# Kernel optimization log

Measured on AMD Instinct MI355X. Metric: run time of the kernel, lower is better.

The kernel has to match this reference:

```python
import jax, jax.numpy as jnp
import numpy as np

B, S, H, F, E, K = 2, 1024, 1024, 4096, 8, 2
TOPK_RATIO = 0.55
EPS = 1e-8


def _ste(x, q):
    # straight-through estimator: forward = q, backward = identity on x
    return x + jax.lax.stop_gradient(q - x)


def ternary_weight(w):
    # BitNet b1.58 absmean ternarization: W -> clip(round(W/mean|W|), -1, 1) * mean|W|
    s = jnp.maximum(jnp.mean(jnp.abs(w)), EPS)
    q = jnp.clip(jnp.round(w / s), -1.0, 1.0) * s
    return _ste(w, q)


def quant_act_int4(x):
    # per-token symmetric int4 fake-quant (range [-7, 7]) with STE
    s = jnp.maximum(jnp.max(jnp.abs(x), axis=-1, keepdims=True), EPS) / 7.0
    q = jnp.clip(jnp.round(x / s), -7.0, 7.0) * s
    return _ste(x, q)


def quant_act_topk_int8(x, ratio):
    # keep top ceil(ratio*d) values by magnitude per token, then int8 fake-quant
    d = x.shape[-1]
    k = int(np.ceil(ratio * d))
    thresh = jax.lax.top_k(jnp.abs(x), k)[0][..., -1:]
    xm = jnp.where(jnp.abs(x) >= thresh, x, 0.0)
    s = jnp.maximum(jnp.max(jnp.abs(xm), axis=-1, keepdims=True), EPS) / 127.0
    q = jnp.clip(jnp.round(xm / s), -127.0, 127.0) * s
    return _ste(xm, q)


def quant_weight_int8(w):
    # per-tensor absmax int8 fake-quant for the router (Int8Linear) with STE
    s = jnp.maximum(jnp.max(jnp.abs(w)), EPS) / 127.0
    q = jnp.clip(jnp.round(w / s), -127.0, 127.0) * s
    return _ste(w, q)


def setup_inputs() -> dict:
    key = jax.random.key(0)
    ks = jax.random.split(key, 5)
    x = jax.random.normal(ks[0], (B, S, H), jnp.float32)
    w_gate = jax.random.normal(ks[1], (E, F, H), jnp.float32) * 0.02
    w_up = jax.random.normal(ks[2], (E, F, H), jnp.float32) * 0.02
    w_down = jax.random.normal(ks[3], (E, H, F), jnp.float32) * 0.02
    w_router = jax.random.normal(ks[4], (E, H), jnp.float32) * 0.02
    return {"x": x, "w_gate": w_gate, "w_up": w_up, "w_down": w_down, "w_router": w_router}


def reference(x, w_gate, w_up, w_down, w_router):
    T = B * S
    xf = x.reshape(T, H)

    # --- router (Int8Linear, higher precision than ternary) ---
    logits = xf @ quant_weight_int8(w_router).T          # [T, E]
    probs = jax.nn.softmax(logits, axis=-1)
    gates, idx = jax.lax.top_k(probs, K)                  # [T, K]
    gates = gates / jnp.sum(gates, axis=-1, keepdims=True)
    # dense combine weights [T, E]
    comb = jnp.zeros((T, E), x.dtype).at[jnp.arange(T)[:, None], idx].set(gates)

    # --- experts: BitFFN (SwiGLU with ternary weights + quantized activations) ---
    xq = quant_act_int4(xf)                               # shared int4 input quant

    def expert(wg, wu, wd):
        g = xq @ ternary_weight(wg).T                     # [T, F]
        u = xq @ ternary_weight(wu).T                     # [T, F]
        h = jax.nn.silu(g) * u
        hq = quant_act_topk_int8(h, TOPK_RATIO)
        return hq @ ternary_weight(wd).T                  # [T, H]

    expert_out = jax.vmap(expert)(w_gate, w_up, w_down)   # [E, T, H]
    out = jnp.einsum('te,eth->th', comb, expert_out)      # gated combine
    return out.reshape(B, S, H)
```

## Files before the change

### kernel.cpp

```cpp
#include <hip/hip_runtime.h>
#include <cstdint>
#include <cstddef>


#define T_TOK 2048
#define HDIM  1024
#define FDIM  4096
#define NEXP  8
#define FH    (FDIM * HDIM)
#define KTOP  2253
#define EPSF  1e-8f
#define PPAD  4608

typedef int v4i  __attribute__((ext_vector_type(4)));
typedef int v16i __attribute__((ext_vector_type(16)));

__global__ __launch_bounds__(256) void k_wabs(const float* __restrict__ w,
                                              float* __restrict__ partials) {
  int m = blockIdx.x, blk = blockIdx.y, tid = threadIdx.x;
  const float4* p = (const float4*)(w + (size_t)m * FH + (size_t)blk * 32768) + tid;
  float s0 = 0.f, s1 = 0.f, s2 = 0.f, s3 = 0.f;
#pragma unroll
  for (int i = 0; i < 8; i++) {
    float4 a = p[(4 * i + 0) * 256];
    float4 b = p[(4 * i + 1) * 256];
    float4 c = p[(4 * i + 2) * 256];
    float4 d = p[(4 * i + 3) * 256];
    s0 += fabsf(a.x) + fabsf(a.y) + fabsf(a.z) + fabsf(a.w);
    s1 += fabsf(b.x) + fabsf(b.y) + fabsf(b.z) + fabsf(b.w);
    s2 += fabsf(c.x) + fabsf(c.y) + fabsf(c.z) + fabsf(c.w);
    s3 += fabsf(d.x) + fabsf(d.y) + fabsf(d.z) + fabsf(d.w);
  }
  float s = (s0 + s1) + (s2 + s3);
  for (int o = 32; o > 0; o >>= 1) s += __shfl_down(s, o);
  __shared__ float lds[4];
  if ((tid & 63) == 0) lds[tid >> 6] = s;
  __syncthreads();
  if (tid == 0) partials[m * 128 + blk] = lds[0] + lds[1] + lds[2] + lds[3];
}

__global__ __launch_bounds__(128) void k_scales8(const float* __restrict__ partials,
                                                 float* __restrict__ s8,
                                                 float* __restrict__ thr8) {
  int tid = threadIdx.x;
  __shared__ float acc[2];
  __shared__ float svals[8];
  for (int m = 0; m < 8; m++) {
    float v = partials[m * 128 + tid];
    for (int o = 32; o > 0; o >>= 1) v += __shfl_down(v, o);
    if ((tid & 63) == 0) acc[tid >> 6] = v;
    __syncthreads();
    if (tid == 0) svals[m] = fmaxf((acc[0] + acc[1]) / (float)FH, EPSF);
    __syncthreads();
  }
  if (tid < 8) {
    float s = svals[tid];
    s8[tid] = s;
    unsigned int lo = 0u, hi = __float_as_uint(s);
    for (int it = 0; it < 32; ++it) {
      unsigned int mid = (lo + hi) >> 1;
      if (mid == lo) break;
      if (__uint_as_float(mid) / s <= 0.5f) lo = mid; else hi = mid;
    }
    thr8[tid] = __uint_as_float(lo);
  }
}

__global__ __launch_bounds__(256) void k_router(const float* __restrict__ wr,
                                                float* __restrict__ wrq) {
  int tid = threadIdx.x;
  __shared__ float lds[4];
  __shared__ float sbc;
  float mx = 0.f;
  for (int i = tid; i < NEXP * HDIM; i += 256) mx = fmaxf(mx, fabsf(wr[i]));
  for (int o = 32; o > 0; o >>= 1) mx = fmaxf(mx, __shfl_down(mx, o));
  if ((tid & 63) == 0) lds[tid >> 6] = mx;
  __syncthreads();
  if (tid == 0)
    sbc = fmaxf(fmaxf(fmaxf(lds[0], lds[1]), fmaxf(lds[2], lds[3])), EPSF) / 127.0f;
  __syncthreads();
  float s = sbc;
  for (int i = tid; i < NEXP * HDIM; i += 256) {
    float q = fminf(fmaxf(rintf(wr[i] / s), -127.f), 127.f);
    wrq[i] = q * s;
  }
}

template <int KD, int RD>
__global__ __launch_bounds__(256) void k_pack(const float* __restrict__ w,
                                              signed char* __restrict__ q,
                                              const float* __restrict__ thr8) {
  constexpr int GR = RD / 32, CCH = KD / 32;
  int e = blockIdx.x / GR, g = blockIdx.x % GR, sl = blockIdx.y;
  float thr = thr8[e];
  __shared__ unsigned int lds[32][257];
  int tid = threadIdx.x;
  const float* wb = w + ((size_t)e * RD + (size_t)g * 32) * KD + (size_t)sl * 1024;
#pragma unroll 4
  for (int i = 0; i < 32; i++) {
    float4 v = *(const float4*)(wb + (size_t)i * KD + tid * 4);
    unsigned int b0 = (fabsf(v.x) > thr) ? ((__float_as_uint(v.x) >> 31) ? 0xFFu : 1u) : 0u;
    unsigned int b1 = (fabsf(v.y) > thr) ? ((__float_as_uint(v.y) >> 31) ? 0xFFu : 1u) : 0u;
    unsigned int b2 = (fabsf(v.z) > thr) ? ((__float_as_uint(v.z) >> 31) ? 0xFFu : 1u) : 0u;
    unsigned int b3 = (fabsf(v.w) > thr) ? ((__float_as_uint(v.w) >> 31) ? 0xFFu : 1u) : 0u;
    lds[i][tid] = b0 | (b1 << 8) | (b2 << 16) | (b3 << 24);
  }
  __syncthreads();
  size_t obase = ((size_t)(e * GR + g) * CCH + (size_t)sl * 32) * 1024;
#pragma unroll
  for (int i2 = 0; i2 < 8; i2++) {
    int mI = i2 * 256 + tid;
    int c = mI >> 6, l2 = mI & 63, ln = l2 & 31, kh = l2 >> 5;
    uint4 d = *(const uint4*)&lds[ln][c * 8 + kh * 4];
    *(uint4*)(q + obase + (size_t)c * 1024 + (size_t)l2 * 16) = d;
  }
}

__global__ __launch_bounds__(256) void k_act_router(const float* __restrict__ x,
                                                    const float* __restrict__ wrq,
                                                    signed char* __restrict__ xq,
                                                    float* __restrict__ sx,
                                                    int* __restrict__ tok_e,
                                                    float* __restrict__ tok_g,
                                                    int* __restrict__ cnt) {
  int t = blockIdx.x, tid = threadIdx.x;
  float4 xv = *(const float4*)(x + (size_t)t * HDIM + tid * 4);
  __shared__ float lds[4];
  __shared__ float sbc;
  __shared__ float part[8][256];
  __shared__ float lg[8];
  float mx = fmaxf(fmaxf(fabsf(xv.x), fabsf(xv.y)), fmaxf(fabsf(xv.z), fabsf(xv.w)));
  for (int o = 32; o > 0; o >>= 1) mx = fmaxf(mx, __shfl_down(mx, o));
  if ((tid & 63) == 0) lds[tid >> 6] = mx;
  __syncthreads();
  if (tid == 0)
    sbc = fmaxf(fmaxf(fmaxf(lds[0], lds[1]), fmaxf(lds[2], lds[3])), EPSF) / 7.0f;
  __syncthreads();
  float s = sbc;
  int q0 = (int)fminf(fmaxf(rintf(xv.x / s), -7.f), 7.f);
  int q1 = (int)fminf(fmaxf(rintf(xv.y / s), -7.f), 7.f);
  int q2 = (int)fminf(fmaxf(rintf(xv.z / s), -7.f), 7.f);
  int q3 = (int)fminf(fmaxf(rintf(xv.w / s), -7.f), 7.f);
  int packed = (q0 & 255) | ((q1 & 255) << 8) | ((q2 & 255) << 16) | (q3 << 24);
  *(int*)(xq + (size_t)t * HDIM + tid * 4) = packed;
  if (tid == 0) sx[t] = s;
#pragma unroll
  for (int e = 0; e < 8; e++) {
    float4 w = *(const float4*)(wrq + e * HDIM + tid * 4);
    part[e][tid] = xv.x * w.x + xv.y * w.y + xv.z * w.z + xv.w * w.w;
  }
  __syncthreads();
  if (tid < 8) {
    float sum = 0.f;
    for (int i = 0; i < 256; i++) sum += part[tid][i];
    lg[tid] = sum;
  }
  __syncthreads();
  if (tid == 0) {
    float m = lg[0];
    for (int e = 1; e < 8; e++) m = fmaxf(m, lg[e]);
    float p[8]; float S = 0.f;
    for (int e = 0; e < 8; e++) { p[e] = expf(lg[e] - m); S += p[e]; }
    for (int e = 0; e < 8; e++) p[e] /= S;
    int e0 = 0;
    for (int e = 1; e < 8; e++) if (p[e] > p[e0]) e0 = e;
    int e1 = -1;
    for (int e = 0; e < 8; e++) { if (e == e0) continue; if (e1 < 0 || p[e] > p[e1]) e1 = e; }
    float g0 = p[e0], g1 = p[e1], gs = g0 + g1;
    tok_e[2 * t] = e0;  tok_e[2 * t + 1] = e1;
    tok_g[2 * t] = g0 / gs;  tok_g[2 * t + 1] = g1 / gs;
    atomicAdd(&cnt[e0], 1); atomicAdd(&cnt[e1], 1);
  }
}

__global__ void k_plan(const int* __restrict__ cnt, int* __restrict__ offs,
                       int* __restrict__ tile_e, int* __restrict__ tile_m0,
                       int* __restrict__ tile_cnt) {
  if (threadIdx.x == 0 && blockIdx.x == 0) {
    int o = 0;
    for (int e = 0; e < 8; e++) { offs[e] = o; o += (cnt[e] + 63) & ~63; }
    offs[8] = o;
    int tt = 0;
    for (int e = 0; e < 8; e++)
      for (int m0 = 0; m0 < cnt[e]; m0 += 64) { tile_e[tt] = e; tile_m0[tt] = m0; tt++; }
    *tile_cnt = tt;
  }
}

__global__ __launch_bounds__(256) void k_scatter(const int* __restrict__ tok_e,
                                                 const float* __restrict__ tok_g,
                                                 const float* __restrict__ sx,
                                                 const int* __restrict__ offs,
                                                 int* __restrict__ cnt2,
                                                 int* __restrict__ pair_tok,
                                                 float* __restrict__ pair_gate,
                                                 float* __restrict__ pair_sx) {
  int t = blockIdx.x * 256 + threadIdx.x;
  if (t >= T_TOK) return;
  for (int k = 0; k < 2; k++) {
    int e = tok_e[2 * t + k];
    int pos = offs[e] + atomicAdd(&cnt2[e], 1);
    pair_tok[pos] = t;
    pair_gate[pos] = tok_g[2 * t + k];
    pair_sx[pos] = sx[t];
  }
}

__global__ __launch_bounds__(256) void k_packA(const int* __restrict__ pair_tok,
                                               const signed char* __restrict__ xq,
                                               signed char* __restrict__ xqp) {
  int idx = blockIdx.x * 256 + threadIdx.x;
  int l = idx & 63, c = (idx >> 6) & 31, pgrp = idx >> 11;
  int p = pgrp * 32 + (l & 31);
  int tok = pair_tok[p];
  const signed char* src = xq + (size_t)tok * HDIM + c * 32 + (l >> 5) * 16;
  *(int4*)(xqp + (size_t)idx * 16) = *(const int4*)src;
}

__global__ __launch_bounds__(256) void k_gemm_gu(const signed char* __restrict__ xqp,
                                                 const signed char* __restrict__ wgp,
                                                 const signed char* __restrict__ wup,
                                                 const int* __restrict__ tile_e,
                                                 const int* __restrict__ tile_m0,
                                                 const int* __restrict__ tile_cnt,
                                                 const int* __restrict__ cnt,
                                                 const int* __restrict__ offs,
                                                 const float* __restrict__ pair_sx,
                                                 const float* __restrict__ s_w,
                                                 unsigned short* __restrict__ hbuf) {
  int bx = blockIdx.x;
  if (bx >= *tile_cnt) return;
  int e = tile_e[bx], m0 = tile_m0[bx];
  int cnt_e = cnt[e], pbase = offs[e];
  int tid = threadIdx.x;
  int wave = tid >> 6, lane = tid & 63, ln = lane & 31, kh = lane >> 5;
  int fgrp = blockIdx.y * 4 + wave;
  const signed char* bg = wgp + (((size_t)e * 128 + fgrp) * 32) * 1024 + lane * 16;
  const signed char* bu = wup + (((size_t)e * 128 + fgrp) * 32) * 1024 + lane * 16;
  const signed char* ap = xqp + ((size_t)((pbase + m0) >> 5) * 32) * 1024 + lane * 16;
  v16i accg0 = {0}, accg1 = {0}, accu0 = {0}, accu1 = {0};
#pragma unroll 8
  for (int c = 0; c < 32; c++) {
    v4i a0 = *(const v4i*)(ap + c * 1024);
    v4i a1 = *(const v4i*)(ap + 32768 + c * 1024);
    v4i b0 = *(const v4i*)(bg + c * 1024);
    v4i b1 = *(const v4i*)(bu + c * 1024);
    accg0 = __builtin_amdgcn_mfma_i32_32x32x32_i8(a0, b0, accg0, 0, 0, 0);
    accg1 = __builtin_amdgcn_mfma_i32_32x32x32_i8(a1, b0, accg1, 0, 0, 0);
    accu0 = __builtin_amdgcn_mfma_i32_32x32x32_i8(a0, b1, accu0, 0, 0, 0);
    accu1 = __builtin_amdgcn_mfma_i32_32x32x32_i8(a1, b1, accu1, 0, 0, 0);
  }
  float sg = s_w[e], su = s_w[8 + e];
  int col = blockIdx.y * 128 + wave * 32 + ln;
#pragma unroll
  for (int r = 0; r < 16; r++) {
    int rr = (r & 3) + 8 * (r >> 2) + 4 * kh;
#pragma unroll
    for (int mt = 0; mt < 2; mt++) {
      int ml = m0 + mt * 32 + rr;
      if (ml < cnt_e) {
        int p = pbase + ml;
        float sxv = pair_sx[p];
        int gi = (mt == 0) ? accg0[r] : accg1[r];
        int ui = (mt == 0) ? accu0[r] : accu1[r];
        float gf = (float)gi * (sxv * sg);
        float uf = (float)ui * (sxv * su);
        float h = gf / (1.0f + expf(-gf)) * uf;
        ((_Float16*)hbuf)[(size_t)p * FDIM + col] = (_Float16)h;
      }
    }
  }
}

__global__ __launch_bounds__(256) void k_select(const unsigned short* __restrict__ hbuf,
                                                signed char* __restrict__ hqp,
                                                const float* __restrict__ pair_gate,
                                                float* __restrict__ pair_f) {
  int wv = threadIdx.x >> 6, lane = threadIdx.x & 63;
  int p = blockIdx.x * 4 + wv;
  const unsigned short* row = hbuf + (size_t)p * FDIM + lane * 64;
  unsigned short hs[64];
#pragma unroll
  for (int i = 0; i < 8; i++)
    *(uint4*)(hs + i * 8) = *(const uint4*)(row + i * 8);
  unsigned short ua[64];
  unsigned int mxb = 0;
#pragma unroll
  for (int j = 0; j < 64; j++) {
    unsigned int u = hs[j] & 0x7fffu;
    ua[j] = (unsigned short)u;
    mxb = (u > mxb) ? u : mxb;
  }
  for (int o = 32; o > 0; o >>= 1) {
    unsigned int t = (unsigned int)__shfl_down((int)mxb, o);
    mxb = (t > mxb) ? t : mxb;
  }
  mxb = (unsigned int)__shfl((int)mxb, 0);
  unsigned int lo = 0, hi = 0x7c00u;
  for (int it = 0; it < 15; ++it) {
    unsigned int mid = (lo + hi) >> 1;
    int cnt = 0;
#pragma unroll
    for (int j = 0; j < 64; j++)
      cnt += (int)__popcll(__ballot((unsigned int)ua[j] >= mid));
    if (cnt >= KTOP) lo = mid; else hi = mid;
  }
  unsigned int thr = lo;
  unsigned short mxs = (unsigned short)mxb;
  float smax = (float)(*(const _Float16*)&mxs);
  float sq = fmaxf(smax, EPSF) / 127.0f;
  int pgrp = p >> 5, ln = p & 31;
#pragma unroll
  for (int gj = 0; gj < 4; gj++) {
    int c = 2 * lane + (gj >> 1);
    int kh = gj & 1;
    signed char outb[16];
#pragma unroll
    for (int t = 0; t < 16; t++) {
      int j = gj * 16 + t;
      float v = (float)(((const _Float16*)hs)[j]);
      float m = ((unsigned int)ua[j] >= thr) ? v : 0.0f;
      float q = fminf(fmaxf(rintf(m / sq), -127.f), 127.f);
      outb[t] = (signed char)(int)q;
    }
    *(int4*)(hqp + ((size_t)((size_t)pgrp * 128 + c) * 64 + kh * 32 + ln) * 16) =
        *(const int4*)outb;
  }
  if (lane == 0) pair_f[p] = pair_gate[p] * sq;
}

__global__ __launch_bounds__(256) void k_gemm_down(const signed char* __restrict__ hqp,
                                                   const signed char* __restrict__ wdp,
                                                   const int* __restrict__ tile_e,
                                                   const int* __restrict__ tile_m0,
                                                   const int* __restrict__ tile_cnt,
                                                   const int* __restrict__ cnt,
                                                   const int* __restrict__ offs,
                                                   const int* __restrict__ pair_tok,
                                                   const float* __restrict__ pair_f,
                                                   const float* __restrict__ s_w,
                                                   float* __restrict__ out) {
  int bx = blockIdx.x;
  if (bx >= *tile_cnt) return;
  int e = tile_e[bx], m0 = tile_m0[bx];
  int cnt_e = cnt[e], pbase = offs[e];
  int tid = threadIdx.x;
  int wave = tid >> 6, lane = tid & 63, ln = lane & 31, kh = lane >> 5;
  int grp_n = blockIdx.y * 4 + wave;
  const signed char* bp = wdp + (((size_t)e * 32 + grp_n) * 128) * 1024 + lane * 16;
  const signed char* ap = hqp + ((size_t)((pbase + m0) >> 5) * 128) * 1024 + lane * 16;
  v16i acc0 = {0}, acc1 = {0};
#pragma unroll 8
  for (int c = 0; c < 128; c++) {
    v4i a0 = *(const v4i*)(ap + (size_t)c * 1024);
    v4i a1 = *(const v4i*)(ap + 131072 + (size_t)c * 1024);
    v4i b  = *(const v4i*)(bp + (size_t)c * 1024);
    acc0 = __builtin_amdgcn_mfma_i32_32x32x32_i8(a0, b, acc0, 0, 0, 0);
    acc1 = __builtin_amdgcn_mfma_i32_32x32x32_i8(a1, b, acc1, 0, 0, 0);
  }
  float sd = s_w[16 + e];
  int col = blockIdx.y * 128 + wave * 32 + ln;
#pragma unroll
  for (int r = 0; r < 16; r++) {
    int rr = (r & 3) + 8 * (r >> 2) + 4 * kh;
#pragma unroll
    for (int mt = 0; mt < 2; mt++) {
      int ml = m0 + mt * 32 + rr;
      if (ml < cnt_e) {
        int p = pbase + ml;
        int ai = (mt == 0) ? acc0[r] : acc1[r];
        float v = (float)ai * (pair_f[p] * sd);
        atomicAdd(out + (size_t)pair_tok[p] * HDIM + col, v);
      }
    }
  }
}

extern "C" void kernel_launch(void* const* d_in, const int* in_sizes, int n_in,
                              void* d_out, int out_size, void* d_ws, size_t ws_size,
                              hipStream_t stream) {
  const float* x  = (const float*)d_in[0];
  const float* wg = (const float*)d_in[1];
  const float* wu = (const float*)d_in[2];
  const float* wd = (const float*)d_in[3];
  const float* wr = (const float*)d_in[4];
  float* out = (float*)d_out;
  char* ws = (char*)d_ws;
  (void)in_sizes; (void)n_in; (void)out_size; (void)ws_size;

  size_t o = 0;
  auto alloc = [&](size_t b) { size_t r = o; o += (b + 255) & ~(size_t)255; return r; };
  float* partials   = (float*)(ws + alloc(3 * 8 * 128 * 4));
  float* s_w        = (float*)(ws + alloc(24 * 4));
  float* thr_w      = (float*)(ws + alloc(24 * 4));
  float* wrq        = (float*)(ws + alloc((size_t)NEXP * HDIM * 4));
  int*   tok_e      = (int*)  (ws + alloc((size_t)T_TOK * 2 * 4));
  float* tok_g      = (float*)(ws + alloc((size_t)T_TOK * 2 * 4));
  int*   cnt        = (int*)  (ws + alloc(256));
  int*   cnt2       = cnt + 8;
  int*   offs       = (int*)  (ws + alloc(16 * 4));
  int*   tile_e     = (int*)  (ws + alloc(128 * 4));
  int*   tile_m0    = (int*)  (ws + alloc(128 * 4));
  int*   tile_cnt   = (int*)  (ws + alloc(4));
  int*   pair_tok   = (int*)  (ws + alloc((size_t)PPAD * 4));
  float* pair_gate  = (float*)(ws + alloc((size_t)PPAD * 4));
  float* pair_sx    = (float*)(ws + alloc((size_t)PPAD * 4));
  float* pair_f     = (float*)(ws + alloc((size_t)PPAD * 4));
  float* sx         = (float*)(ws + alloc((size_t)T_TOK * 4));
  signed char* xq   = (signed char*)(ws + alloc((size_t)T_TOK * HDIM));
  signed char* xqp  = (signed char*)(ws + alloc((size_t)PPAD * HDIM));
  signed char* wgp  = (signed char*)(ws + alloc((size_t)NEXP * FH));
  signed char* wup  = (signed char*)(ws + alloc((size_t)NEXP * FH));
  signed char* wdp  = (signed char*)(ws + alloc((size_t)NEXP * FH));
  unsigned short* hbuf = (unsigned short*)(ws + alloc((size_t)PPAD * FDIM * 2));
  signed char* hqp  = (signed char*)(ws + alloc((size_t)PPAD * FDIM));

  hipMemsetAsync(cnt, 0, 64, stream);
  hipMemsetAsync(pair_tok, 0, (size_t)PPAD * 4, stream);
  hipMemsetAsync(out, 0, (size_t)T_TOK * HDIM * 4, stream);

  k_wabs<<<dim3(8, 128), 256, 0, stream>>>(wg, partials);
  k_scales8<<<1, 128, 0, stream>>>(partials, s_w, thr_w);
  k_pack<1024, 4096><<<dim3(1024, 1), 256, 0, stream>>>(wg, wgp, thr_w);

  k_wabs<<<dim3(8, 128), 256, 0, stream>>>(wu, partials + 1024);
  k_scales8<<<1, 128, 0, stream>>>(partials + 1024, s_w + 8, thr_w + 8);
  k_pack<1024, 4096><<<dim3(1024, 1), 256, 0, stream>>>(wu, wup, thr_w + 8);

  k_wabs<<<dim3(8, 128), 256, 0, stream>>>(wd, partials + 2048);
  k_scales8<<<1, 128, 0, stream>>>(partials + 2048, s_w + 16, thr_w + 16);
  k_pack<4096, 1024><<<dim3(256, 4), 256, 0, stream>>>(wd, wdp, thr_w + 16);

  k_router<<<1, 256, 0, stream>>>(wr, wrq);
  k_act_router<<<T_TOK, 256, 0, stream>>>(x, wrq, xq, sx, tok_e, tok_g, cnt);
  k_plan<<<1, 64, 0, stream>>>(cnt, offs, tile_e, tile_m0, tile_cnt);
  k_scatter<<<8, 256, 0, stream>>>(tok_e, tok_g, sx, offs, cnt2, pair_tok, pair_gate, pair_sx);
  k_packA<<<PPAD / 4, 256, 0, stream>>>(pair_tok, xq, xqp);
  k_gemm_gu<<<dim3(72, 32), 256, 0, stream>>>(xqp, wgp, wup, tile_e, tile_m0, tile_cnt,
                                              cnt, offs, pair_sx, s_w, hbuf);
  k_select<<<PPAD / 4, 256, 0, stream>>>(hbuf, hqp, pair_gate, pair_f);
  k_gemm_down<<<dim3(72, 8), 256, 0, stream>>>(hqp, wdp, tile_e, tile_m0, tile_cnt,
                                               cnt, offs, pair_tok, pair_f, s_w, out);
}
```

Baseline: 810.5 us.

## Enlarge MoE GEMM row tiles to 128 tokens and split down-proj K

```diff
diff --git a/kernel.cpp b/kernel.cpp
--- a/kernel.cpp
+++ b/kernel.cpp
@@ -10,7 +10,7 @@
 #define FH    (FDIM * HDIM)
 #define KTOP  2253
 #define EPSF  1e-8f
-#define PPAD  4608
+#define PPAD  5120
 
 typedef int v4i  __attribute__((ext_vector_type(4)));
 typedef int v16i __attribute__((ext_vector_type(16)));
@@ -178,11 +178,11 @@
                        int* __restrict__ tile_cnt) {
   if (threadIdx.x == 0 && blockIdx.x == 0) {
     int o = 0;
-    for (int e = 0; e < 8; e++) { offs[e] = o; o += (cnt[e] + 63) & ~63; }
+    for (int e = 0; e < 8; e++) { offs[e] = o; o += (cnt[e] + 127) & ~127; }
     offs[8] = o;
     int tt = 0;
     for (int e = 0; e < 8; e++)
-      for (int m0 = 0; m0 < cnt[e]; m0 += 64) { tile_e[tt] = e; tile_m0[tt] = m0; tt++; }
+      for (int m0 = 0; m0 < cnt[e]; m0 += 128) { tile_e[tt] = e; tile_m0[tt] = m0; tt++; }
     *tile_cnt = tt;
   }
 }
@@ -217,17 +217,17 @@
   *(int4*)(xqp + (size_t)idx * 16) = *(const int4*)src;
 }
 
-__global__ __launch_bounds__(256) void k_gemm_gu(const signed char* __restrict__ xqp,
-                                                 const signed char* __restrict__ wgp,
-                                                 const signed char* __restrict__ wup,
-                                                 const int* __restrict__ tile_e,
-                                                 const int* __restrict__ tile_m0,
-                                                 const int* __restrict__ tile_cnt,
-                                                 const int* __restrict__ cnt,
-                                                 const int* __restrict__ offs,
-                                                 const float* __restrict__ pair_sx,
-                                                 const float* __restrict__ s_w,
-                                                 unsigned short* __restrict__ hbuf) {
+__global__ __launch_bounds__(256, 2) void k_gemm_gu(const signed char* __restrict__ xqp,
+                                                    const signed char* __restrict__ wgp,
+                                                    const signed char* __restrict__ wup,
+                                                    const int* __restrict__ tile_e,
+                                                    const int* __restrict__ tile_m0,
+                                                    const int* __restrict__ tile_cnt,
+                                                    const int* __restrict__ cnt,
+                                                    const int* __restrict__ offs,
+                                                    const float* __restrict__ pair_sx,
+                                                    const float* __restrict__ s_w,
+                                                    unsigned short* __restrict__ hbuf) {
   int bx = blockIdx.x;
   if (bx >= *tile_cnt) return;
   int e = tile_e[bx], m0 = tile_m0[bx];
@@ -238,33 +238,34 @@
   const signed char* bg = wgp + (((size_t)e * 128 + fgrp) * 32) * 1024 + lane * 16;
   const signed char* bu = wup + (((size_t)e * 128 + fgrp) * 32) * 1024 + lane * 16;
   const signed char* ap = xqp + ((size_t)((pbase + m0) >> 5) * 32) * 1024 + lane * 16;
-  v16i accg0 = {0}, accg1 = {0}, accu0 = {0}, accu1 = {0};
-#pragma unroll 8
+  v16i acc[4][2] = {};
+#pragma unroll 2
   for (int c = 0; c < 32; c++) {
-    v4i a0 = *(const v4i*)(ap + c * 1024);
-    v4i a1 = *(const v4i*)(ap + 32768 + c * 1024);
-    v4i b0 = *(const v4i*)(bg + c * 1024);
-    v4i b1 = *(const v4i*)(bu + c * 1024);
-    accg0 = __builtin_amdgcn_mfma_i32_32x32x32_i8(a0, b0, accg0, 0, 0, 0);
-    accg1 = __builtin_amdgcn_mfma_i32_32x32x32_i8(a1, b0, accg1, 0, 0, 0);
-    accu0 = __builtin_amdgcn_mfma_i32_32x32x32_i8(a0, b1, accu0, 0, 0, 0);
-    accu1 = __builtin_amdgcn_mfma_i32_32x32x32_i8(a1, b1, accu1, 0, 0, 0);
+    v4i a[4];
+#pragma unroll
+    for (int mg = 0; mg < 4; mg++)
+      a[mg] = *(const v4i*)(ap + (size_t)(mg * 32 + c) * 1024);
+    v4i b0 = *(const v4i*)(bg + (size_t)c * 1024);
+    v4i b1 = *(const v4i*)(bu + (size_t)c * 1024);
+#pragma unroll
+    for (int mg = 0; mg < 4; mg++) {
+      acc[mg][0] = __builtin_amdgcn_mfma_i32_32x32x32_i8(a[mg], b0, acc[mg][0], 0, 0, 0);
+      acc[mg][1] = __builtin_amdgcn_mfma_i32_32x32x32_i8(a[mg], b1, acc[mg][1], 0, 0, 0);
+    }
   }
   float sg = s_w[e], su = s_w[8 + e];
   int col = blockIdx.y * 128 + wave * 32 + ln;
 #pragma unroll
-  for (int r = 0; r < 16; r++) {
-    int rr = (r & 3) + 8 * (r >> 2) + 4 * kh;
-#pragma unroll
-    for (int mt = 0; mt < 2; mt++) {
-      int ml = m0 + mt * 32 + rr;
+  for (int mg = 0; mg < 4; mg++) {
+#pragma unroll
+    for (int r = 0; r < 16; r++) {
+      int rr = (r & 3) + 8 * (r >> 2) + 4 * kh;
+      int ml = m0 + mg * 32 + rr;
       if (ml < cnt_e) {
         int p = pbase + ml;
         float sxv = pair_sx[p];
-        int gi = (mt == 0) ? accg0[r] : accg1[r];
-        int ui = (mt == 0) ? accu0[r] : accu1[r];
-        float gf = (float)gi * (sxv * sg);
-        float uf = (float)ui * (sxv * su);
+        float gf = (float)acc[mg][0][r] * (sxv * sg);
+        float uf = (float)acc[mg][1][r] * (sxv * su);
         float h = gf / (1.0f + expf(-gf)) * uf;
         ((_Float16*)hbuf)[(size_t)p * FDIM + col] = (_Float16)h;
       }
@@ -299,11 +300,11 @@
   unsigned int lo = 0, hi = 0x7c00u;
   for (int it = 0; it < 15; ++it) {
     unsigned int mid = (lo + hi) >> 1;
-    int cnt = 0;
+    int cntk = 0;
 #pragma unroll
     for (int j = 0; j < 64; j++)
-      cnt += (int)__popcll(__ballot((unsigned int)ua[j] >= mid));
-    if (cnt >= KTOP) lo = mid; else hi = mid;
+      cntk += (int)__popcll(__ballot((unsigned int)ua[j] >= mid));
+    if (cntk >= KTOP) lo = mid; else hi = mid;
   }
   unsigned int thr = lo;
   unsigned short mxs = (unsigned short)mxb;
@@ -329,47 +330,50 @@
   if (lane == 0) pair_f[p] = pair_gate[p] * sq;
 }
 
-__global__ __launch_bounds__(256) void k_gemm_down(const signed char* __restrict__ hqp,
-                                                   const signed char* __restrict__ wdp,
-                                                   const int* __restrict__ tile_e,
-                                                   const int* __restrict__ tile_m0,
-                                                   const int* __restrict__ tile_cnt,
-                                                   const int* __restrict__ cnt,
-                                                   const int* __restrict__ offs,
-                                                   const int* __restrict__ pair_tok,
-                                                   const float* __restrict__ pair_f,
-                                                   const float* __restrict__ s_w,
-                                                   float* __restrict__ out) {
+__global__ __launch_bounds__(256, 2) void k_gemm_down(const signed char* __restrict__ hqp,
+                                                      const signed char* __restrict__ wdp,
+                                                      const int* __restrict__ tile_e,
+                                                      const int* __restrict__ tile_m0,
+                                                      const int* __restrict__ tile_cnt,
+                                                      const int* __restrict__ cnt,
+                                                      const int* __restrict__ offs,
+                                                      const int* __restrict__ pair_tok,
+                                                      const float* __restrict__ pair_f,
+                                                      const float* __restrict__ s_w,
+                                                      float* __restrict__ out) {
   int bx = blockIdx.x;
   if (bx >= *tile_cnt) return;
   int e = tile_e[bx], m0 = tile_m0[bx];
   int cnt_e = cnt[e], pbase = offs[e];
   int tid = threadIdx.x;
   int wave = tid >> 6, lane = tid & 63, ln = lane & 31, kh = lane >> 5;
-  int grp_n = blockIdx.y * 4 + wave;
-  const signed char* bp = wdp + (((size_t)e * 32 + grp_n) * 128) * 1024 + lane * 16;
+  int ggrp = blockIdx.y * 4 + wave;
+  int c0 = blockIdx.z * 64;
+  const signed char* bp = wdp + (((size_t)e * 32 + ggrp) * 128) * 1024 + lane * 16;
   const signed char* ap = hqp + ((size_t)((pbase + m0) >> 5) * 128) * 1024 + lane * 16;
-  v16i acc0 = {0}, acc1 = {0};
-#pragma unroll 8
-  for (int c = 0; c < 128; c++) {
-    v4i a0 = *(const v4i*)(ap + (size_t)c * 1024);
-    v4i a1 = *(const v4i*)(ap + 131072 + (size_t)c * 1024);
-    v4i b  = *(const v4i*)(bp + (size_t)c * 1024);
-    acc0 = __builtin_amdgcn_mfma_i32_32x32x32_i8(a0, b, acc0, 0, 0, 0);
-    acc1 = __builtin_amdgcn_mfma_i32_32x32x32_i8(a1, b, acc1, 0, 0, 0);
+  v16i acc[4] = {};
+#pragma unroll 4
+  for (int c = c0; c < c0 + 64; c++) {
+    v4i a[4];
+#pragma unroll
+    for (int mg = 0; mg < 4; mg++)
+      a[mg] = *(const v4i*)(ap + (size_t)(mg * 128 + c) * 1024);
+    v4i b = *(const v4i*)(bp + (size_t)c * 1024);
+#pragma unroll
+    for (int mg = 0; mg < 4; mg++)
+      acc[mg] = __builtin_amdgcn_mfma_i32_32x32x32_i8(a[mg], b, acc[mg], 0, 0, 0);
   }
   float sd = s_w[16 + e];
   int col = blockIdx.y * 128 + wave * 32 + ln;
 #pragma unroll
-  for (int r = 0; r < 16; r++) {
-    int rr = (r & 3) + 8 * (r >> 2) + 4 * kh;
-#pragma unroll
-    for (int mt = 0; mt < 2; mt++) {
-      int ml = m0 + mt * 32 + rr;
+  for (int mg = 0; mg < 4; mg++) {
+#pragma unroll
+    for (int r = 0; r < 16; r++) {
+      int rr = (r & 3) + 8 * (r >> 2) + 4 * kh;
+      int ml = m0 + mg * 32 + rr;
       if (ml < cnt_e) {
         int p = pbase + ml;
-        int ai = (mt == 0) ? acc0[r] : acc1[r];
-        float v = (float)ai * (pair_f[p] * sd);
+        float v = (float)acc[mg][r] * (pair_f[p] * sd);
         atomicAdd(out + (size_t)pair_tok[p] * HDIM + col, v);
       }
     }
@@ -436,9 +440,9 @@
   k_plan<<<1, 64, 0, stream>>>(cnt, offs, tile_e, tile_m0, tile_cnt);
   k_scatter<<<8, 256, 0, stream>>>(tok_e, tok_g, sx, offs, cnt2, pair_tok, pair_gate, pair_sx);
   k_packA<<<PPAD / 4, 256, 0, stream>>>(pair_tok, xq, xqp);
-  k_gemm_gu<<<dim3(72, 32), 256, 0, stream>>>(xqp, wgp, wup, tile_e, tile_m0, tile_cnt,
+  k_gemm_gu<<<dim3(40, 32), 256, 0, stream>>>(xqp, wgp, wup, tile_e, tile_m0, tile_cnt,
                                               cnt, offs, pair_sx, s_w, hbuf);
   k_select<<<PPAD / 4, 256, 0, stream>>>(hbuf, hqp, pair_gate, pair_f);
-  k_gemm_down<<<dim3(72, 8), 256, 0, stream>>>(hqp, wdp, tile_e, tile_m0, tile_cnt,
-                                               cnt, offs, pair_tok, pair_f, s_w, out);
-}
+  k_gemm_down<<<dim3(40, 8, 2), 256, 0, stream>>>(hqp, wdp, tile_e, tile_m0, tile_cnt,
+                                                  cnt, offs, pair_tok, pair_f, s_w, out);
+}
```

Result: no change. 818.7 us (+1.0%).
